# Performance work log

Hardware: AMD Instinct MI355X
Metric: run time of the kernel (lower is better)

Reference implementation:

```python
import jax, jax.numpy as jnp
import numpy as np

EPS = 1e-6


def _rmsnorm(x, weight, eps=EPS):
    # float32 compute, cast back to input dtype, then scale (matches torch module)
    xf = x.astype(jnp.float32)
    rms = jax.lax.rsqrt(jnp.mean(xf * xf, axis=-1, keepdims=True) + eps)
    return (xf * rms).astype(x.dtype) * weight


def _block_attn_res(V, pseudo_query, norm_weight):
    # V: [n, b, t, d]; pseudo_query, norm_weight: [d]
    K = _rmsnorm(V, norm_weight)                          # [n,b,t,d]
    d = pseudo_query.shape[-1]
    logits = jnp.einsum('d,nbtd->nbt', pseudo_query, K) / jnp.sqrt(jnp.float32(d))
    attn = jax.nn.softmax(logits, axis=0)                 # softmax over block axis n
    return jnp.einsum('nbt,nbtd->btd', attn, V)           # [b,t,d]


def setup_inputs() -> dict:
    key = jax.random.key(0)
    ks = jax.random.split(key, 4)
    N, B, T, D = 7, 2, 4096, 2048
    return {
        'blocks': jax.random.normal(ks[0], (N, B, T, D), dtype=jnp.float32),
        'partial_block': jax.random.normal(ks[1], (B, T, D), dtype=jnp.float32),
        'pseudo_query_attn': jax.random.normal(ks[2], (D,), dtype=jnp.float32),
        'pseudo_query_mlp': jax.random.normal(ks[3], (D,), dtype=jnp.float32),
        'norm_weight_attn': jnp.ones((D,), dtype=jnp.float32),
        'norm_weight_mlp': jnp.ones((D,), dtype=jnp.float32),
    }


def reference(blocks, partial_block, pseudo_query_attn, pseudo_query_mlp,
              norm_weight_attn, norm_weight_mlp):
    # V = stack(blocks + [partial_block], dim=0): [N+1, B, T, D]
    V = jnp.concatenate([blocks, partial_block[None]], axis=0)
    h_attn = _block_attn_res(V, pseudo_query_attn, norm_weight_attn)
    h_mlp = _block_attn_res(V, pseudo_query_mlp, norm_weight_mlp)
    return (h_attn, h_mlp)
```

## Files before the change

kernel.cpp:

```cpp
#include <hip/hip_runtime.h>

#define NB 8
#define DDIM 2048
#define THREADS 512
#define NWAVES (THREADS / 64)

typedef float f32x4 __attribute__((ext_vector_type(4)));

__device__ __forceinline__ float wave_sum64(float x) {
    int t;
    t = __builtin_amdgcn_update_dpp(0, __float_as_int(x), 0x111, 0xf, 0xf, false);
    x += __int_as_float(t);
    t = __builtin_amdgcn_update_dpp(0, __float_as_int(x), 0x112, 0xf, 0xf, false);
    x += __int_as_float(t);
    t = __builtin_amdgcn_update_dpp(0, __float_as_int(x), 0x114, 0xf, 0xf, false);
    x += __int_as_float(t);
    t = __builtin_amdgcn_update_dpp(0, __float_as_int(x), 0x118, 0xf, 0xf, false);
    x += __int_as_float(t);
    t = __builtin_amdgcn_update_dpp(0, __float_as_int(x), 0x142, 0xa, 0xf, false);
    x += __int_as_float(t);
    t = __builtin_amdgcn_update_dpp(0, __float_as_int(x), 0x143, 0xc, 0xf, false);
    x += __int_as_float(t);
    return x;
}

__global__ __launch_bounds__(THREADS, 6)
void block_attn_res_kernel(
    const float* __restrict__ blocks,
    const float* __restrict__ partial,
    const float* __restrict__ qa,
    const float* __restrict__ qm,
    const float* __restrict__ wa,
    const float* __restrict__ wm,
    float* __restrict__ out,
    int BT)
{
    const int row = blockIdx.x;
    const int tid = threadIdx.x;
    const int c   = tid * 4;

    const size_t rowBase = (size_t)row * DDIM;
    const size_t nStride = (size_t)BT * DDIM;

    __shared__ float red[NWAVES * 24];

    f32x4 v[NB];
    {
        const float* base = blocks + rowBase + c;
#pragma unroll
        for (int n = 0; n < NB - 1; ++n)
            v[n] = *reinterpret_cast<const f32x4*>(base + (size_t)n * nStride);
        v[NB - 1] = *reinterpret_cast<const f32x4*>(partial + rowBase + c);
    }

    const f32x4 qwa = *reinterpret_cast<const f32x4*>(qa + c) *
                      *reinterpret_cast<const f32x4*>(wa + c);
    const f32x4 qwm = *reinterpret_cast<const f32x4*>(qm + c) *
                      *reinterpret_cast<const f32x4*>(wm + c);

    const int wave = tid >> 6;
    const bool is63 = (tid & 63) == 63;
#pragma unroll
    for (int n = 0; n < NB; ++n) {
        float s = 0.f, pa = 0.f, pm = 0.f;
#pragma unroll
        for (int j = 0; j < 4; ++j) {
            s  += v[n][j] * v[n][j];
            pa += qwa[j]  * v[n][j];
            pm += qwm[j]  * v[n][j];
        }
        s  = wave_sum64(s);
        pa = wave_sum64(pa);
        pm = wave_sum64(pm);
        if (is63) {
            red[wave * 24 + n]      = s;
            red[wave * 24 + 8 + n]  = pa;
            red[wave * 24 + 16 + n] = pm;
        }
    }
    __syncthreads();

    float t24[24];
    {
        const f32x4* r4 = reinterpret_cast<const f32x4*>(red);
#pragma unroll
        for (int g = 0; g < 6; ++g) {
            f32x4 x = r4[g];
#pragma unroll
            for (int w = 1; w < NWAVES; ++w) x += r4[w * 6 + g];
            t24[4 * g + 0] = x.x; t24[4 * g + 1] = x.y;
            t24[4 * g + 2] = x.z; t24[4 * g + 3] = x.w;
        }
    }

    const float inv_sqrt_d = rsqrtf((float)DDIM);
    float lga[NB], lgm[NB];
#pragma unroll
    for (int n = 0; n < NB; ++n) {
        float rms = rsqrtf(t24[n] * (1.0f / DDIM) + 1e-6f);
        lga[n] = t24[8 + n]  * rms * inv_sqrt_d;
        lgm[n] = t24[16 + n] * rms * inv_sqrt_d;
    }
    float ma = lga[0], mm = lgm[0];
#pragma unroll
    for (int n = 1; n < NB; ++n) { ma = fmaxf(ma, lga[n]); mm = fmaxf(mm, lgm[n]); }

    f32x4 oa = (f32x4)(0.f), om = (f32x4)(0.f);
    float sa = 0.f, sm = 0.f;
#pragma unroll
    for (int n = 0; n < NB; ++n) {
        float ea = __expf(lga[n] - ma); sa += ea; oa += ea * v[n];
        float em = __expf(lgm[n] - mm); sm += em; om += em * v[n];
    }
    oa *= (1.f / sa);
    om *= (1.f / sm);

    __builtin_nontemporal_store(oa, reinterpret_cast<f32x4*>(out + rowBase + c));
    __builtin_nontemporal_store(om, reinterpret_cast<f32x4*>(out + nStride + rowBase + c));
}

extern "C" void kernel_launch(void* const* d_in, const int* in_sizes, int n_in,
                              void* d_out, int out_size, void* d_ws, size_t ws_size,
                              hipStream_t stream)
{
    const float* blocks  = (const float*)d_in[0];
    const float* partial = (const float*)d_in[1];
    const float* qa      = (const float*)d_in[2];
    const float* qm      = (const float*)d_in[3];
    const float* wa      = (const float*)d_in[4];
    const float* wm      = (const float*)d_in[5];
    float* out = (float*)d_out;

    const int D  = in_sizes[2];
    const int BT = in_sizes[1] / D;

    dim3 grid(BT), block(THREADS);
    hipLaunchKernelGGL(block_attn_res_kernel, grid, block, 0, stream,
                       blocks, partial, qa, qm, wa, wm, out, BT);
}
```

Baseline: 124.1 us.

## Halve block size, give each thread two vectors, and compute softmax weights in one wave

Each row is now handled by 256 threads instead of 512, and each thread loads two float4 chunks per block. The cross-wave reduction and softmax are done once by the first wave, and the normalized weights are shared with the other threads through shared memory. The aim is to cut redundant per-thread softmax work and reduction overhead and to put more loads in flight per thread. In exchange, register pressure roughly doubles, the launch-bounds occupancy hint drops from 6 to 4, and an extra barrier is added.

After: 122.2 us. No clear change (-1.5%).

```diff
diff --git a/kernel.cpp b/kernel.cpp
--- a/kernel.cpp
+++ b/kernel.cpp
@@ -2,7 +2,7 @@
 
 #define NB 8
 #define DDIM 2048
-#define THREADS 512
+#define THREADS 256
 #define NWAVES (THREADS / 64)
 
 typedef float f32x4 __attribute__((ext_vector_type(4)));
@@ -24,7 +24,7 @@
     return x;
 }
 
-__global__ __launch_bounds__(THREADS, 6)
+__global__ __launch_bounds__(THREADS, 4)
 void block_attn_res_kernel(
     const float* __restrict__ blocks,
     const float* __restrict__ partial,
@@ -37,26 +37,32 @@
 {
     const int row = blockIdx.x;
     const int tid = threadIdx.x;
-    const int c   = tid * 4;
+    const int c0 = tid * 4;
+    const int c1 = c0 + DDIM / 2;
 
     const size_t rowBase = (size_t)row * DDIM;
     const size_t nStride = (size_t)BT * DDIM;
 
     __shared__ float red[NWAVES * 24];
+    __shared__ float wgt[16];
 
-    f32x4 v[NB];
-    {
-        const float* base = blocks + rowBase + c;
+    f32x4 v[NB][2];
 #pragma unroll
-        for (int n = 0; n < NB - 1; ++n)
-            v[n] = *reinterpret_cast<const f32x4*>(base + (size_t)n * nStride);
-        v[NB - 1] = *reinterpret_cast<const f32x4*>(partial + rowBase + c);
+    for (int n = 0; n < NB; ++n) {
+        const float* src = (n < NB - 1) ? (blocks + (size_t)n * nStride + rowBase)
+                                        : (partial + rowBase);
+        v[n][0] = *reinterpret_cast<const f32x4*>(src + c0);
+        v[n][1] = *reinterpret_cast<const f32x4*>(src + c1);
     }
 
-    const f32x4 qwa = *reinterpret_cast<const f32x4*>(qa + c) *
-                      *reinterpret_cast<const f32x4*>(wa + c);
-    const f32x4 qwm = *reinterpret_cast<const f32x4*>(qm + c) *
-                      *reinterpret_cast<const f32x4*>(wm + c);
+    const f32x4 qwa0 = *reinterpret_cast<const f32x4*>(qa + c0) *
+                       *reinterpret_cast<const f32x4*>(wa + c0);
+    const f32x4 qwa1 = *reinterpret_cast<const f32x4*>(qa + c1) *
+                       *reinterpret_cast<const f32x4*>(wa + c1);
+    const f32x4 qwm0 = *reinterpret_cast<const f32x4*>(qm + c0) *
+                       *reinterpret_cast<const f32x4*>(wm + c0);
+    const f32x4 qwm1 = *reinterpret_cast<const f32x4*>(qm + c1) *
+                       *reinterpret_cast<const f32x4*>(wm + c1);
 
     const int wave = tid >> 6;
     const bool is63 = (tid & 63) == 63;
@@ -65,9 +71,9 @@
         float s = 0.f, pa = 0.f, pm = 0.f;
 #pragma unroll
         for (int j = 0; j < 4; ++j) {
-            s  += v[n][j] * v[n][j];
-            pa += qwa[j]  * v[n][j];
-            pm += qwm[j]  * v[n][j];
+            s  += v[n][0][j] * v[n][0][j] + v[n][1][j] * v[n][1][j];
+            pa += qwa0[j] * v[n][0][j] + qwa1[j] * v[n][1][j];
+            pm += qwm0[j] * v[n][0][j] + qwm1[j] * v[n][1][j];
         }
         s  = wave_sum64(s);
         pa = wave_sum64(pa);
@@ -80,43 +86,70 @@
     }
     __syncthreads();
 
-    float t24[24];
-    {
-        const f32x4* r4 = reinterpret_cast<const f32x4*>(red);
+    if (tid < 64) {
+        float t24[24];
+        {
+            const f32x4* r4 = reinterpret_cast<const f32x4*>(red);
 #pragma unroll
-        for (int g = 0; g < 6; ++g) {
-            f32x4 x = r4[g];
+            for (int g = 0; g < 6; ++g) {
+                f32x4 x = r4[g] + r4[6 + g] + r4[12 + g] + r4[18 + g];
+                t24[4 * g + 0] = x.x; t24[4 * g + 1] = x.y;
+                t24[4 * g + 2] = x.z; t24[4 * g + 3] = x.w;
+            }
+        }
+        const float inv_sqrt_d = rsqrtf((float)DDIM);
+        float lga[NB], lgm[NB];
 #pragma unroll
-            for (int w = 1; w < NWAVES; ++w) x += r4[w * 6 + g];
-            t24[4 * g + 0] = x.x; t24[4 * g + 1] = x.y;
-            t24[4 * g + 2] = x.z; t24[4 * g + 3] = x.w;
+        for (int n = 0; n < NB; ++n) {
+            float rms = rsqrtf(t24[n] * (1.0f / DDIM) + 1e-6f);
+            lga[n] = t24[8 + n]  * rms * inv_sqrt_d;
+            lgm[n] = t24[16 + n] * rms * inv_sqrt_d;
+        }
+        float ma = lga[0], mm = lgm[0];
+#pragma unroll
+        for (int n = 1; n < NB; ++n) { ma = fmaxf(ma, lga[n]); mm = fmaxf(mm, lgm[n]); }
+        float aw[NB], mw[NB];
+        float sa = 0.f, sm = 0.f;
+#pragma unroll
+        for (int n = 0; n < NB; ++n) {
+            aw[n] = __expf(lga[n] - ma); sa += aw[n];
+            mw[n] = __expf(lgm[n] - mm); sm += mw[n];
+        }
+        const float ra = 1.f / sa, rm = 1.f / sm;
+        if (tid == 0) {
+            f32x4* w4 = reinterpret_cast<f32x4*>(wgt);
+            w4[0] = (f32x4){aw[0] * ra, aw[1] * ra, aw[2] * ra, aw[3] * ra};
+            w4[1] = (f32x4){aw[4] * ra, aw[5] * ra, aw[6] * ra, aw[7] * ra};
+            w4[2] = (f32x4){mw[0] * rm, mw[1] * rm, mw[2] * rm, mw[3] * rm};
+            w4[3] = (f32x4){mw[4] * rm, mw[5] * rm, mw[6] * rm, mw[7] * rm};
         }
     }
+    __syncthreads();
 
-    const float inv_sqrt_d = rsqrtf((float)DDIM);
-    float lga[NB], lgm[NB];
+    float awn[NB], mwn[NB];
+    {
+        const f32x4* w4 = reinterpret_cast<const f32x4*>(wgt);
+        f32x4 a0 = w4[0], a1 = w4[1], m0 = w4[2], m1 = w4[3];
+        awn[0] = a0.x; awn[1] = a0.y; awn[2] = a0.z; awn[3] = a0.w;
+        awn[4] = a1.x; awn[5] = a1.y; awn[6] = a1.z; awn[7] = a1.w;
+        mwn[0] = m0.x; mwn[1] = m0.y; mwn[2] = m0.z; mwn[3] = m0.w;
+        mwn[4] = m1.x; mwn[5] = m1.y; mwn[6] = m1.z; mwn[7] = m1.w;
+    }
+
+    f32x4 oa0 = (f32x4)(0.f), oa1 = (f32x4)(0.f);
+    f32x4 om0 = (f32x4)(0.f), om1 = (f32x4)(0.f);
 #pragma unroll
     for (int n = 0; n < NB; ++n) {
-        float rms = rsqrtf(t24[n] * (1.0f / DDIM) + 1e-6f);
-        lga[n] = t24[8 + n]  * rms * inv_sqrt_d;
-        lgm[n] = t24[16 + n] * rms * inv_sqrt_d;
+        oa0 += awn[n] * v[n][0]; oa1 += awn[n] * v[n][1];
+        om0 += mwn[n] * v[n][0]; om1 += mwn[n] * v[n][1];
     }
-    float ma = lga[0], mm = lgm[0];
-#pragma unroll
-    for (int n = 1; n < NB; ++n) { ma = fmaxf(ma, lga[n]); mm = fmaxf(mm, lgm[n]); }
 
-    f32x4 oa = (f32x4)(0.f), om = (f32x4)(0.f);
-    float sa = 0.f, sm = 0.f;
-#pragma unroll
-    for (int n = 0; n < NB; ++n) {
-        float ea = __expf(lga[n] - ma); sa += ea; oa += ea * v[n];
-        float em = __expf(lgm[n] - mm); sm += em; om += em * v[n];
-    }
-    oa *= (1.f / sa);
-    om *= (1.f / sm);
-
-    __builtin_nontemporal_store(oa, reinterpret_cast<f32x4*>(out + rowBase + c));
-    __builtin_nontemporal_store(om, reinterpret_cast<f32x4*>(out + nStride + rowBase + c));
+    float* outa = out + rowBase;
+    float* outm = out + nStride + rowBase;
+    __builtin_nontemporal_store(oa0, reinterpret_cast<f32x4*>(outa + c0));
+    __builtin_nontemporal_store(oa1, reinterpret_cast<f32x4*>(outa + c1));
+    __builtin_nontemporal_store(om0, reinterpret_cast<f32x4*>(outm + c0));
+    __builtin_nontemporal_store(om1, reinterpret_cast<f32x4*>(outm + c1));
 }
 
 extern "C" void kernel_launch(void* const* d_in, const int* in_sizes, int n_in,
```
